# Kernel tuning notes

Hardware: AMD Instinct MI355X
Metric: run time of the kernel (lower is better)

## Reference

```python
import jax, jax.numpy as jnp
import numpy as np

N_NODES = 100000
N_EDGES = 3200000
IN_F = 256
OUT_F = 128


def setup_inputs() -> dict:
    key = jax.random.key(0)
    k1, k2, k3, k4, k5, k6 = jax.random.split(key, 6)
    x = jax.random.normal(k1, (N_NODES, IN_F), dtype=jnp.float32)
    edge_row = jax.random.randint(k2, (N_EDGES,), 0, N_NODES, dtype=jnp.int32)
    edge_col = jax.random.randint(k3, (N_EDGES,), 0, N_NODES, dtype=jnp.int32)
    edge_val = jax.random.uniform(k4, (N_EDGES,), dtype=jnp.float32)
    # xavier_uniform with relu gain, as in reset_parameters
    gain = float(np.sqrt(2.0))
    bound = gain * float(np.sqrt(6.0 / (IN_F + OUT_F)))
    w = jax.random.uniform(k5, (IN_F, OUT_F), minval=-bound, maxval=bound, dtype=jnp.float32)
    std = 1.0 / float(np.sqrt(OUT_F))
    bias = jax.random.uniform(k6, (OUT_F,), minval=-std, maxval=std, dtype=jnp.float32)
    return {"x": x, "edge_row": edge_row, "edge_col": edge_col,
            "edge_val": edge_val, "w": w, "bias": bias}


def reference(x, edge_row, edge_col, edge_val, w, bias):
    # h = x @ w : dense feature transform [N, out]
    h = jnp.matmul(x, w)
    # spmm(adj, h): out[r] = sum_e adj_val[e] * h[c[e]] for edges e with row r
    msgs = edge_val[:, None] * h[edge_col]  # [E, out]
    agg = jax.ops.segment_sum(msgs, edge_row, num_segments=N_NODES)
    return agg + bias
```

## Files before the change

### kernel.cpp

```cpp
#include <hip/hip_runtime.h>
#include <hip/hip_bf16.h>

#define N_NODES 100000
#define N_EDGES 3200000
#define IN_F 256
#define OUT_F 128

#define NBIN 391
#define NBC  800
#define CHUNK 4000
#define GEMM_BLOCKS 782

typedef __attribute__((ext_vector_type(8))) short bf16x8;
typedef __attribute__((ext_vector_type(4))) float f32x4;

union U4BF { uint4 u; bf16x8 v; };

__device__ inline unsigned short f2bf(float f) {
    return __bfloat16_as_ushort(__float2bfloat16(f));
}
__device__ inline unsigned pk2(float a, float b) {
    unsigned la = __bfloat16_as_ushort(__float2bfloat16(a));
    unsigned lb = __bfloat16_as_ushort(__float2bfloat16(b));
    return la | (lb << 16);
}

__global__ __launch_bounds__(256) void conv_w_kernel(
    const float* __restrict__ w, uint4* __restrict__ wbfF)
{
    int tid = blockIdx.x * 256 + threadIdx.x;
    int ks = tid >> 9;
    int fn = (tid >> 6) & 7;
    int l  = tid & 63;
    int c  = fn * 16 + (l & 15);
    int k0 = ks * 32 + (l >> 4) * 8;
    const float* wp = w + (size_t)k0 * OUT_F + c;
    uint4 u;
    u.x = pk2(wp[0 * OUT_F], wp[1 * OUT_F]);
    u.y = pk2(wp[2 * OUT_F], wp[3 * OUT_F]);
    u.z = pk2(wp[4 * OUT_F], wp[5 * OUT_F]);
    u.w = pk2(wp[6 * OUT_F], wp[7 * OUT_F]);
    wbfF[tid] = u;
}

__global__ __launch_bounds__(256) void gemm_hist_kernel(
    const float* __restrict__ x, const uint4* __restrict__ wbfF,
    unsigned short* __restrict__ h,
    const int* __restrict__ erow, int* __restrict__ cntmat)
{
    __shared__ __align__(16) char smem[65536];
    const int t = threadIdx.x;

    if (blockIdx.x < GEMM_BLOCKS) {
        uint4* bsh = (uint4*)smem;
        const int lane = t & 63;
        const int wid  = t >> 6;
        const int brow = blockIdx.x * 128;
        const int ln   = lane & 15;
        const int kb   = lane >> 4;

#pragma unroll
        for (int i = 0; i < 16; ++i) bsh[i * 256 + t] = wbfF[i * 256 + t];

        int r0 = brow + wid * 32 + ln;
        int r1 = r0 + 16;
        const float* a0p = x + (size_t)(r0 < N_NODES ? r0 : N_NODES - 1) * IN_F;
        const float* a1p = x + (size_t)(r1 < N_NODES ? r1 : N_NODES - 1) * IN_F;

        f32x4 acc[2][8] = {};
        __syncthreads();

#pragma unroll
        for (int ks = 0; ks < 8; ++ks) {
            const int k = ks * 32 + kb * 8;
            U4BF a0, a1;
            {
                float4 p = *(const float4*)(a0p + k);
                float4 q = *(const float4*)(a0p + k + 4);
                a0.u.x = pk2(p.x, p.y); a0.u.y = pk2(p.z, p.w);
                a0.u.z = pk2(q.x, q.y); a0.u.w = pk2(q.z, q.w);
            }
            {
                float4 p = *(const float4*)(a1p + k);
                float4 q = *(const float4*)(a1p + k + 4);
                a1.u.x = pk2(p.x, p.y); a1.u.y = pk2(p.z, p.w);
                a1.u.z = pk2(q.x, q.y); a1.u.w = pk2(q.z, q.w);
            }
            U4BF b[8];
#pragma unroll
            for (int fn = 0; fn < 8; ++fn)
                b[fn].u = bsh[(ks * 8 + fn) * 64 + lane];
#pragma unroll
            for (int fn = 0; fn < 8; ++fn) {
                acc[0][fn] = __builtin_amdgcn_mfma_f32_16x16x32_bf16(
                    a0.v, b[fn].v, acc[0][fn], 0, 0, 0);
                acc[1][fn] = __builtin_amdgcn_mfma_f32_16x16x32_bf16(
                    a1.v, b[fn].v, acc[1][fn], 0, 0, 0);
            }
        }

#pragma unroll
        for (int fm = 0; fm < 2; ++fm) {
#pragma unroll
            for (int r = 0; r < 4; ++r) {
                int grow = brow + wid * 32 + fm * 16 + (lane >> 4) * 4 + r;
                if (grow < N_NODES) {
                    unsigned short* dst = h + (size_t)grow * OUT_F + ln;
#pragma unroll
                    for (int fn = 0; fn < 8; ++fn)
                        dst[fn * 16] = f2bf(acc[fm][fn][r]);
                }
            }
        }
    } else {
        int* lhist = (int*)smem;
        const int b = blockIdx.x - GEMM_BLOCKS;
        for (int i = t; i < NBIN; i += 256) lhist[i] = 0;
        __syncthreads();

        const int base = b * CHUNK;
        const int end  = min(base + CHUNK, N_EDGES);
        for (int i = base + t * 4; i < end; i += 1024) {
            int4 r = *(const int4*)(erow + i);
            atomicAdd(&lhist[r.x >> 8], 1);
            atomicAdd(&lhist[r.y >> 8], 1);
            atomicAdd(&lhist[r.z >> 8], 1);
            atomicAdd(&lhist[r.w >> 8], 1);
        }
        __syncthreads();

        int* dst = cntmat + (size_t)b * NBIN;
        for (int j = t; j < NBIN; j += 256) dst[j] = lhist[j];
    }
}

__global__ __launch_bounds__(256) void pass_b_kernel(
    const int* __restrict__ cntmat, int* __restrict__ blockbase,
    int* __restrict__ tot)
{
    __shared__ int sh[256];
    const int t = threadIdx.x;
    const int j = blockIdx.x;
    int c[4];
    int ps = 0;
#pragma unroll
    for (int i = 0; i < 4; ++i) {
        int bb = 4 * t + i;
        c[i] = (bb < NBC) ? cntmat[(size_t)bb * NBIN + j] : 0;
        ps += c[i];
    }
    sh[t] = ps;
    __syncthreads();
    for (int off = 1; off < 256; off <<= 1) {
        int add = (t >= off) ? sh[t - off] : 0;
        __syncthreads();
        sh[t] += add;
        __syncthreads();
    }
    int excl = sh[t] - ps;
#pragma unroll
    for (int i = 0; i < 4; ++i) {
        int bb = 4 * t + i;
        if (bb < NBC) { blockbase[(size_t)bb * NBIN + j] = excl; excl += c[i]; }
    }
    if (t == 255) tot[j] = sh[255];
}

__global__ __launch_bounds__(512) void pass_b2_kernel(
    const int* __restrict__ tot, int* __restrict__ bucket_base)
{
    __shared__ int sh[512];
    const int t = threadIdx.x;
    int v = (t < NBIN) ? tot[t] : 0;
    sh[t] = v;
    __syncthreads();
    for (int off = 1; off < 512; off <<= 1) {
        int add = (t >= off) ? sh[t - off] : 0;
        __syncthreads();
        sh[t] += add;
        __syncthreads();
    }
    if (t < NBIN + 1) bucket_base[t] = sh[t] - v;
}

__global__ __launch_bounds__(256) void pass_c_kernel(
    const int* __restrict__ erow, const int* __restrict__ ecol,
    const float* __restrict__ eval_, const int* __restrict__ cntmat,
    const int* __restrict__ blockbase, const int* __restrict__ bucket_base,
    int2* __restrict__ tmp)
{
    __shared__ int2 skv[CHUNK];
    __shared__ int  sdelta[CHUNK];
    __shared__ int  cur[NBIN];
    __shared__ int  sdel[NBIN];
    __shared__ int  sscan[256];

    const int t = threadIdx.x;
    const int b = blockIdx.x;

    int j0 = 2 * t, j1 = 2 * t + 1;
    int c0 = (j0 < NBIN) ? cntmat[(size_t)b * NBIN + j0] : 0;
    int c1 = (j1 < NBIN) ? cntmat[(size_t)b * NBIN + j1] : 0;
    int ps = c0 + c1;
    sscan[t] = ps;
    __syncthreads();
    for (int off = 1; off < 256; off <<= 1) {
        int add = (t >= off) ? sscan[t - off] : 0;
        __syncthreads();
        sscan[t] += add;
        __syncthreads();
    }
    int excl = sscan[t] - ps;
    if (j0 < NBIN) {
        cur[j0]  = excl;
        sdel[j0] = bucket_base[j0] + blockbase[(size_t)b * NBIN + j0] - excl;
    }
    if (j1 < NBIN) {
        cur[j1]  = excl + c0;
        sdel[j1] = bucket_base[j1] + blockbase[(size_t)b * NBIN + j1] - (excl + c0);
    }
    __syncthreads();

    const int base = b * CHUNK;
    const int end  = min(base + CHUNK, N_EDGES);
    for (int i = base + t * 4; i < end; i += 1024) {
        int4   r = *(const int4*)(erow + i);
        int4   c = *(const int4*)(ecol + i);
        float4 v = *(const float4*)(eval_ + i);
        int bin, pos;
        bin = r.x >> 8; pos = atomicAdd(&cur[bin], 1);
        skv[pos] = make_int2(c.x | ((r.x & 255) << 17), __float_as_int(v.x));
        sdelta[pos] = sdel[bin];
        bin = r.y >> 8; pos = atomicAdd(&cur[bin], 1);
        skv[pos] = make_int2(c.y | ((r.y & 255) << 17), __float_as_int(v.y));
        sdelta[pos] = sdel[bin];
        bin = r.z >> 8; pos = atomicAdd(&cur[bin], 1);
        skv[pos] = make_int2(c.z | ((r.z & 255) << 17), __float_as_int(v.z));
        sdelta[pos] = sdel[bin];
        bin = r.w >> 8; pos = atomicAdd(&cur[bin], 1);
        skv[pos] = make_int2(c.w | ((r.w & 255) << 17), __float_as_int(v.w));
        sdelta[pos] = sdel[bin];
    }
    __syncthreads();

    const int n = end - base;
    for (int i = t; i < n; i += 256) {
        int2 kv = skv[i];
        tmp[sdelta[i] + i] = kv;
    }
}

__global__ __launch_bounds__(256) void pass_d_kernel(
    const int2* __restrict__ tmp, const int* __restrict__ bucket_base,
    int2* __restrict__ packed, int* __restrict__ row_start,
    int* __restrict__ rowtot)
{
    __shared__ int hist[256];
    __shared__ int cursor[256];
    const int t = threadIdx.x;
    const int j = blockIdx.x;
    const int base = bucket_base[j];
    const int end  = bucket_base[j + 1];

    hist[t] = 0;
    __syncthreads();

    for (int i = base + t; i < end; i += 256)
        atomicAdd(&hist[tmp[i].x >> 17], 1);
    __syncthreads();

    int hv = hist[t];
    cursor[t] = hv;
    __syncthreads();
    for (int off = 1; off < 256; off <<= 1) {
        int add = (t >= off) ? cursor[t - off] : 0;
        __syncthreads();
        cursor[t] += add;
        __syncthreads();
    }
    int excl = cursor[t] - hv;

    int r = j * 256 + t;
    if (r < N_NODES) {
        row_start[r] = base + excl;
        rowtot[r]    = hv;
    }
    __syncthreads();
    cursor[t] = excl;
    __syncthreads();

    for (int i = base + t; i < end; i += 256) {
        int2 p = tmp[i];
        int rl = p.x >> 17;
        int pos = atomicAdd(&cursor[rl], 1);
        packed[base + pos] = make_int2(p.x & 0x1FFFF, p.y);
    }
}

__global__ __launch_bounds__(256) void aggregate_kernel(
    const int2* __restrict__ packed, const int* __restrict__ row_start,
    const int* __restrict__ rowtot, const unsigned* __restrict__ h2,
    const float* __restrict__ bias, float* __restrict__ out)
{
    int wave = (blockIdx.x * 256 + threadIdx.x) >> 6;
    int lane = threadIdx.x & 63;
    if (wave >= N_NODES) return;

    int start = __builtin_amdgcn_readfirstlane(row_start[wave]);
    int deg   = __builtin_amdgcn_readfirstlane(rowtot[wave]);
    int end   = start + deg;

    const unsigned* hb = h2 + lane;
    float ax = 0.f, ay = 0.f;

    int e = start;
    for (; e + 7 < end; e += 8) {
        int2 p0 = packed[e];
        int2 p1 = packed[e + 1];
        int2 p2 = packed[e + 2];
        int2 p3 = packed[e + 3];
        int2 p4 = packed[e + 4];
        int2 p5 = packed[e + 5];
        int2 p6 = packed[e + 6];
        int2 p7 = packed[e + 7];
        unsigned u0 = hb[(size_t)p0.x << 6];
        unsigned u1 = hb[(size_t)p1.x << 6];
        unsigned u2 = hb[(size_t)p2.x << 6];
        unsigned u3 = hb[(size_t)p3.x << 6];
        unsigned u4 = hb[(size_t)p4.x << 6];
        unsigned u5 = hb[(size_t)p5.x << 6];
        unsigned u6 = hb[(size_t)p6.x << 6];
        unsigned u7 = hb[(size_t)p7.x << 6];
        float v0 = __int_as_float(p0.y), v1 = __int_as_float(p1.y);
        float v2 = __int_as_float(p2.y), v3 = __int_as_float(p3.y);
        float v4 = __int_as_float(p4.y), v5 = __int_as_float(p5.y);
        float v6 = __int_as_float(p6.y), v7 = __int_as_float(p7.y);
        ax = fmaf(v0, __uint_as_float(u0 << 16), ax);
        ay = fmaf(v0, __uint_as_float(u0 & 0xFFFF0000u), ay);
        ax = fmaf(v1, __uint_as_float(u1 << 16), ax);
        ay = fmaf(v1, __uint_as_float(u1 & 0xFFFF0000u), ay);
        ax = fmaf(v2, __uint_as_float(u2 << 16), ax);
        ay = fmaf(v2, __uint_as_float(u2 & 0xFFFF0000u), ay);
        ax = fmaf(v3, __uint_as_float(u3 << 16), ax);
        ay = fmaf(v3, __uint_as_float(u3 & 0xFFFF0000u), ay);
        ax = fmaf(v4, __uint_as_float(u4 << 16), ax);
        ay = fmaf(v4, __uint_as_float(u4 & 0xFFFF0000u), ay);
        ax = fmaf(v5, __uint_as_float(u5 << 16), ax);
        ay = fmaf(v5, __uint_as_float(u5 & 0xFFFF0000u), ay);
        ax = fmaf(v6, __uint_as_float(u6 << 16), ax);
        ay = fmaf(v6, __uint_as_float(u6 & 0xFFFF0000u), ay);
        ax = fmaf(v7, __uint_as_float(u7 << 16), ax);
        ay = fmaf(v7, __uint_as_float(u7 & 0xFFFF0000u), ay);
    }
    for (; e < end; ++e) {
        int2 p0 = packed[e];
        unsigned u0 = hb[(size_t)p0.x << 6];
        float v0 = __int_as_float(p0.y);
        ax = fmaf(v0, __uint_as_float(u0 << 16), ax);
        ay = fmaf(v0, __uint_as_float(u0 & 0xFFFF0000u), ay);
    }

    float2 b = *(const float2*)(bias + lane * 2);
    *(float2*)(out + (size_t)wave * OUT_F + lane * 2) = make_float2(ax + b.x, ay + b.y);
}

extern "C" void kernel_launch(void* const* d_in, const int* in_sizes, int n_in,
                              void* d_out, int out_size, void* d_ws, size_t ws_size,
                              hipStream_t stream)
{
    const float* x     = (const float*)d_in[0];
    const int*   erow  = (const int*)d_in[1];
    const int*   ecol  = (const int*)d_in[2];
    const float* eval_ = (const float*)d_in[3];
    const float* w     = (const float*)d_in[4];
    const float* bias  = (const float*)d_in[5];
    float*       out   = (float*)d_out;

    char* ws = (char*)d_ws;
    unsigned short* h           = (unsigned short*)(ws);
    int2*           tmp         = (int2*)(ws + 25600000);
    int2*           packed      = (int2*)(ws + 51200000);
    int*            cntmat      = (int*)(ws + 76800000);
    int*            blockbase   = (int*)(ws + 78051200);
    int*            tot         = (int*)(ws + 79302400);
    int*            bucket_base = (int*)(ws + 79303968);
    int*            row_start   = (int*)(ws + 79305536);
    int*            rowtot      = (int*)(ws + 79705536);
    uint4*          wbfF        = (uint4*)(ws + 80105536);

    hipLaunchKernelGGL(conv_w_kernel, dim3(16), dim3(256), 0, stream, w, wbfF);

    hipLaunchKernelGGL(gemm_hist_kernel, dim3(GEMM_BLOCKS + NBC), dim3(256), 0, stream,
                       x, wbfF, h, erow, cntmat);

    hipLaunchKernelGGL(pass_b_kernel, dim3(NBIN), dim3(256), 0, stream,
                       cntmat, blockbase, tot);
    hipLaunchKernelGGL(pass_b2_kernel, dim3(1), dim3(512), 0, stream, tot, bucket_base);

    hipLaunchKernelGGL(pass_c_kernel, dim3(NBC), dim3(256), 0, stream,
                       erow, ecol, eval_, cntmat, blockbase, bucket_base, tmp);

    hipLaunchKernelGGL(pass_d_kernel, dim3(NBIN), dim3(256), 0, stream,
                       tmp, bucket_base, packed, row_start, rowtot);

    hipLaunchKernelGGL(aggregate_kernel,
                       dim3((N_NODES * 64 + 255) / 256), dim3(256), 0, stream,
                       packed, row_start, rowtot, (const unsigned*)h, bias, out);
}
```

Measured before the change: 216.9 us.

## Fuse per-bucket row sort with aggregation using 64-row LDS buckets

The row-bucket width drops from 256 to 64 rows, with bin counts, chunk sizes and scan kernels resized to match. The final per-row counting sort and the SpMM aggregation are merged into one kernel. That kernel sorts each bucket's edges into LDS and gathers h rows straight from there, so the packed edge array and the row_start/rowtot arrays are no longer written to or read from global memory. The trade-offs are a fixed LDS capacity of 4096 edges per bucket with no overflow guard, and more bins in the histogram and scatter passes.

```diff
diff --git a/kernel.cpp b/kernel.cpp
--- a/kernel.cpp
+++ b/kernel.cpp
@@ -6,10 +6,13 @@
 #define IN_F 256
 #define OUT_F 128
 
-#define NBIN 391
-#define NBC  800
-#define CHUNK 4000
+#define RPB 64
+#define NBIN 1563
+#define NBC  1000
+#define CHUNK 3200
 #define GEMM_BLOCKS 782
+#define BPT 7
+#define CAP 4096
 
 typedef __attribute__((ext_vector_type(8))) short bf16x8;
 typedef __attribute__((ext_vector_type(4))) float f32x4;
@@ -122,10 +125,10 @@
         const int end  = min(base + CHUNK, N_EDGES);
         for (int i = base + t * 4; i < end; i += 1024) {
             int4 r = *(const int4*)(erow + i);
-            atomicAdd(&lhist[r.x >> 8], 1);
-            atomicAdd(&lhist[r.y >> 8], 1);
-            atomicAdd(&lhist[r.z >> 8], 1);
-            atomicAdd(&lhist[r.w >> 8], 1);
+            atomicAdd(&lhist[r.x >> 6], 1);
+            atomicAdd(&lhist[r.y >> 6], 1);
+            atomicAdd(&lhist[r.z >> 6], 1);
+            atomicAdd(&lhist[r.w >> 6], 1);
         }
         __syncthreads();
 
@@ -166,21 +169,26 @@
     if (t == 255) tot[j] = sh[255];
 }
 
-__global__ __launch_bounds__(512) void pass_b2_kernel(
+__global__ __launch_bounds__(1024) void pass_b2_kernel(
     const int* __restrict__ tot, int* __restrict__ bucket_base)
 {
-    __shared__ int sh[512];
+    __shared__ int sh[1024];
     const int t = threadIdx.x;
-    int v = (t < NBIN) ? tot[t] : 0;
-    sh[t] = v;
-    __syncthreads();
-    for (int off = 1; off < 512; off <<= 1) {
+    const int i0 = 2 * t, i1 = 2 * t + 1;
+    int v0 = (i0 < NBIN) ? tot[i0] : 0;
+    int v1 = (i1 < NBIN) ? tot[i1] : 0;
+    int ps = v0 + v1;
+    sh[t] = ps;
+    __syncthreads();
+    for (int off = 1; off < 1024; off <<= 1) {
         int add = (t >= off) ? sh[t - off] : 0;
         __syncthreads();
         sh[t] += add;
         __syncthreads();
     }
-    if (t < NBIN + 1) bucket_base[t] = sh[t] - v;
+    int excl = sh[t] - ps;
+    if (i0 <= NBIN) bucket_base[i0] = excl;
+    if (i1 <= NBIN) bucket_base[i1] = excl + v0;
 }
 
 __global__ __launch_bounds__(256) void pass_c_kernel(
@@ -190,7 +198,7 @@
     int2* __restrict__ tmp)
 {
     __shared__ int2 skv[CHUNK];
-    __shared__ int  sdelta[CHUNK];
+    __shared__ unsigned short sbin[CHUNK];
     __shared__ int  cur[NBIN];
     __shared__ int  sdel[NBIN];
     __shared__ int  sscan[256];
@@ -198,10 +206,14 @@
     const int t = threadIdx.x;
     const int b = blockIdx.x;
 
-    int j0 = 2 * t, j1 = 2 * t + 1;
-    int c0 = (j0 < NBIN) ? cntmat[(size_t)b * NBIN + j0] : 0;
-    int c1 = (j1 < NBIN) ? cntmat[(size_t)b * NBIN + j1] : 0;
-    int ps = c0 + c1;
+    int c[BPT];
+    int ps = 0;
+#pragma unroll
+    for (int i = 0; i < BPT; ++i) {
+        int bin = t * BPT + i;
+        c[i] = (bin < NBIN) ? cntmat[(size_t)b * NBIN + bin] : 0;
+        ps += c[i];
+    }
     sscan[t] = ps;
     __syncthreads();
     for (int off = 1; off < 256; off <<= 1) {
@@ -211,13 +223,14 @@
         __syncthreads();
     }
     int excl = sscan[t] - ps;
-    if (j0 < NBIN) {
-        cur[j0]  = excl;
-        sdel[j0] = bucket_base[j0] + blockbase[(size_t)b * NBIN + j0] - excl;
-    }
-    if (j1 < NBIN) {
-        cur[j1]  = excl + c0;
-        sdel[j1] = bucket_base[j1] + blockbase[(size_t)b * NBIN + j1] - (excl + c0);
+#pragma unroll
+    for (int i = 0; i < BPT; ++i) {
+        int bin = t * BPT + i;
+        if (bin < NBIN) {
+            cur[bin]  = excl;
+            sdel[bin] = bucket_base[bin] + blockbase[(size_t)b * NBIN + bin] - excl;
+            excl += c[i];
+        }
     }
     __syncthreads();
 
@@ -225,143 +238,132 @@
     const int end  = min(base + CHUNK, N_EDGES);
     for (int i = base + t * 4; i < end; i += 1024) {
         int4   r = *(const int4*)(erow + i);
-        int4   c = *(const int4*)(ecol + i);
+        int4   cc = *(const int4*)(ecol + i);
         float4 v = *(const float4*)(eval_ + i);
         int bin, pos;
-        bin = r.x >> 8; pos = atomicAdd(&cur[bin], 1);
-        skv[pos] = make_int2(c.x | ((r.x & 255) << 17), __float_as_int(v.x));
-        sdelta[pos] = sdel[bin];
-        bin = r.y >> 8; pos = atomicAdd(&cur[bin], 1);
-        skv[pos] = make_int2(c.y | ((r.y & 255) << 17), __float_as_int(v.y));
-        sdelta[pos] = sdel[bin];
-        bin = r.z >> 8; pos = atomicAdd(&cur[bin], 1);
-        skv[pos] = make_int2(c.z | ((r.z & 255) << 17), __float_as_int(v.z));
-        sdelta[pos] = sdel[bin];
-        bin = r.w >> 8; pos = atomicAdd(&cur[bin], 1);
-        skv[pos] = make_int2(c.w | ((r.w & 255) << 17), __float_as_int(v.w));
-        sdelta[pos] = sdel[bin];
+        bin = r.x >> 6; pos = atomicAdd(&cur[bin], 1);
+        skv[pos] = make_int2(cc.x | ((r.x & 63) << 17), __float_as_int(v.x));
+        sbin[pos] = (unsigned short)bin;
+        bin = r.y >> 6; pos = atomicAdd(&cur[bin], 1);
+        skv[pos] = make_int2(cc.y | ((r.y & 63) << 17), __float_as_int(v.y));
+        sbin[pos] = (unsigned short)bin;
+        bin = r.z >> 6; pos = atomicAdd(&cur[bin], 1);
+        skv[pos] = make_int2(cc.z | ((r.z & 63) << 17), __float_as_int(v.z));
+        sbin[pos] = (unsigned short)bin;
+        bin = r.w >> 6; pos = atomicAdd(&cur[bin], 1);
+        skv[pos] = make_int2(cc.w | ((r.w & 63) << 17), __float_as_int(v.w));
+        sbin[pos] = (unsigned short)bin;
     }
     __syncthreads();
 
     const int n = end - base;
     for (int i = t; i < n; i += 256) {
         int2 kv = skv[i];
-        tmp[sdelta[i] + i] = kv;
-    }
-}
-
-__global__ __launch_bounds__(256) void pass_d_kernel(
+        tmp[sdel[sbin[i]] + i] = kv;
+    }
+}
+
+__global__ __launch_bounds__(512) void fused_da_kernel(
     const int2* __restrict__ tmp, const int* __restrict__ bucket_base,
-    int2* __restrict__ packed, int* __restrict__ row_start,
-    int* __restrict__ rowtot)
-{
-    __shared__ int hist[256];
-    __shared__ int cursor[256];
-    const int t = threadIdx.x;
-    const int j = blockIdx.x;
+    const unsigned* __restrict__ h2, const float* __restrict__ bias,
+    float* __restrict__ out)
+{
+    __shared__ int2 skv[CAP];
+    __shared__ int  srow[RPB];
+    __shared__ int  scnt[RPB];
+    __shared__ int  cursor[RPB];
+
+    const int t    = threadIdx.x;
+    const int lane = t & 63;
+    const int w    = t >> 6;
+    const int j    = blockIdx.x;
     const int base = bucket_base[j];
-    const int end  = bucket_base[j + 1];
-
-    hist[t] = 0;
-    __syncthreads();
-
-    for (int i = base + t; i < end; i += 256)
-        atomicAdd(&hist[tmp[i].x >> 17], 1);
-    __syncthreads();
-
-    int hv = hist[t];
-    cursor[t] = hv;
-    __syncthreads();
-    for (int off = 1; off < 256; off <<= 1) {
-        int add = (t >= off) ? cursor[t - off] : 0;
-        __syncthreads();
-        cursor[t] += add;
-        __syncthreads();
-    }
-    int excl = cursor[t] - hv;
-
-    int r = j * 256 + t;
-    if (r < N_NODES) {
-        row_start[r] = base + excl;
-        rowtot[r]    = hv;
-    }
-    __syncthreads();
-    cursor[t] = excl;
-    __syncthreads();
-
-    for (int i = base + t; i < end; i += 256) {
-        int2 p = tmp[i];
+    const int n    = bucket_base[j + 1] - base;
+
+    if (t < RPB) cursor[t] = 0;
+    __syncthreads();
+    for (int i = t; i < n; i += 512)
+        atomicAdd(&cursor[tmp[base + i].x >> 17], 1);
+    __syncthreads();
+    if (t < RPB) { scnt[t] = cursor[t]; srow[t] = cursor[t]; }
+    __syncthreads();
+    for (int off = 1; off < RPB; off <<= 1) {
+        int add = (t >= off && t < RPB) ? srow[t - off] : 0;
+        __syncthreads();
+        if (t < RPB) srow[t] += add;
+        __syncthreads();
+    }
+    if (t < RPB) { int ex = srow[t] - scnt[t]; srow[t] = ex; cursor[t] = ex; }
+    __syncthreads();
+
+    for (int i = t; i < n; i += 512) {
+        int2 p = tmp[base + i];
         int rl = p.x >> 17;
         int pos = atomicAdd(&cursor[rl], 1);
-        packed[base + pos] = make_int2(p.x & 0x1FFFF, p.y);
-    }
-}
-
-__global__ __launch_bounds__(256) void aggregate_kernel(
-    const int2* __restrict__ packed, const int* __restrict__ row_start,
-    const int* __restrict__ rowtot, const unsigned* __restrict__ h2,
-    const float* __restrict__ bias, float* __restrict__ out)
-{
-    int wave = (blockIdx.x * 256 + threadIdx.x) >> 6;
-    int lane = threadIdx.x & 63;
-    if (wave >= N_NODES) return;
-
-    int start = __builtin_amdgcn_readfirstlane(row_start[wave]);
-    int deg   = __builtin_amdgcn_readfirstlane(rowtot[wave]);
-    int end   = start + deg;
+        skv[pos] = make_int2(p.x & 0x1FFFF, p.y);
+    }
+    __syncthreads();
 
     const unsigned* hb = h2 + lane;
-    float ax = 0.f, ay = 0.f;
-
-    int e = start;
-    for (; e + 7 < end; e += 8) {
-        int2 p0 = packed[e];
-        int2 p1 = packed[e + 1];
-        int2 p2 = packed[e + 2];
-        int2 p3 = packed[e + 3];
-        int2 p4 = packed[e + 4];
-        int2 p5 = packed[e + 5];
-        int2 p6 = packed[e + 6];
-        int2 p7 = packed[e + 7];
-        unsigned u0 = hb[(size_t)p0.x << 6];
-        unsigned u1 = hb[(size_t)p1.x << 6];
-        unsigned u2 = hb[(size_t)p2.x << 6];
-        unsigned u3 = hb[(size_t)p3.x << 6];
-        unsigned u4 = hb[(size_t)p4.x << 6];
-        unsigned u5 = hb[(size_t)p5.x << 6];
-        unsigned u6 = hb[(size_t)p6.x << 6];
-        unsigned u7 = hb[(size_t)p7.x << 6];
-        float v0 = __int_as_float(p0.y), v1 = __int_as_float(p1.y);
-        float v2 = __int_as_float(p2.y), v3 = __int_as_float(p3.y);
-        float v4 = __int_as_float(p4.y), v5 = __int_as_float(p5.y);
-        float v6 = __int_as_float(p6.y), v7 = __int_as_float(p7.y);
-        ax = fmaf(v0, __uint_as_float(u0 << 16), ax);
-        ay = fmaf(v0, __uint_as_float(u0 & 0xFFFF0000u), ay);
-        ax = fmaf(v1, __uint_as_float(u1 << 16), ax);
-        ay = fmaf(v1, __uint_as_float(u1 & 0xFFFF0000u), ay);
-        ax = fmaf(v2, __uint_as_float(u2 << 16), ax);
-        ay = fmaf(v2, __uint_as_float(u2 & 0xFFFF0000u), ay);
-        ax = fmaf(v3, __uint_as_float(u3 << 16), ax);
-        ay = fmaf(v3, __uint_as_float(u3 & 0xFFFF0000u), ay);
-        ax = fmaf(v4, __uint_as_float(u4 << 16), ax);
-        ay = fmaf(v4, __uint_as_float(u4 & 0xFFFF0000u), ay);
-        ax = fmaf(v5, __uint_as_float(u5 << 16), ax);
-        ay = fmaf(v5, __uint_as_float(u5 & 0xFFFF0000u), ay);
-        ax = fmaf(v6, __uint_as_float(u6 << 16), ax);
-        ay = fmaf(v6, __uint_as_float(u6 & 0xFFFF0000u), ay);
-        ax = fmaf(v7, __uint_as_float(u7 << 16), ax);
-        ay = fmaf(v7, __uint_as_float(u7 & 0xFFFF0000u), ay);
-    }
-    for (; e < end; ++e) {
-        int2 p0 = packed[e];
-        unsigned u0 = hb[(size_t)p0.x << 6];
-        float v0 = __int_as_float(p0.y);
-        ax = fmaf(v0, __uint_as_float(u0 << 16), ax);
-        ay = fmaf(v0, __uint_as_float(u0 & 0xFFFF0000u), ay);
-    }
-
-    float2 b = *(const float2*)(bias + lane * 2);
-    *(float2*)(out + (size_t)wave * OUT_F + lane * 2) = make_float2(ax + b.x, ay + b.y);
+#pragma unroll 1
+    for (int rr = w * 8; rr < w * 8 + 8; ++rr) {
+        int gr = j * RPB + rr;
+        if (gr >= N_NODES) break;
+        int s = srow[rr];
+        int end = s + scnt[rr];
+        float ax = 0.f, ay = 0.f;
+
+        int e = s;
+        for (; e + 7 < end; e += 8) {
+            int2 p0 = skv[e];
+            int2 p1 = skv[e + 1];
+            int2 p2 = skv[e + 2];
+            int2 p3 = skv[e + 3];
+            int2 p4 = skv[e + 4];
+            int2 p5 = skv[e + 5];
+            int2 p6 = skv[e + 6];
+            int2 p7 = skv[e + 7];
+            unsigned u0 = hb[(size_t)p0.x << 6];
+            unsigned u1 = hb[(size_t)p1.x << 6];
+            unsigned u2 = hb[(size_t)p2.x << 6];
+            unsigned u3 = hb[(size_t)p3.x << 6];
+            unsigned u4 = hb[(size_t)p4.x << 6];
+            unsigned u5 = hb[(size_t)p5.x << 6];
+            unsigned u6 = hb[(size_t)p6.x << 6];
+            unsigned u7 = hb[(size_t)p7.x << 6];
+            float v0 = __int_as_float(p0.y), v1 = __int_as_float(p1.y);
+            float v2 = __int_as_float(p2.y), v3 = __int_as_float(p3.y);
+            float v4 = __int_as_float(p4.y), v5 = __int_as_float(p5.y);
+            float v6 = __int_as_float(p6.y), v7 = __int_as_float(p7.y);
+            ax = fmaf(v0, __uint_as_float(u0 << 16), ax);
+            ay = fmaf(v0, __uint_as_float(u0 & 0xFFFF0000u), ay);
+            ax = fmaf(v1, __uint_as_float(u1 << 16), ax);
+            ay = fmaf(v1, __uint_as_float(u1 & 0xFFFF0000u), ay);
+            ax = fmaf(v2, __uint_as_float(u2 << 16), ax);
+            ay = fmaf(v2, __uint_as_float(u2 & 0xFFFF0000u), ay);
+            ax = fmaf(v3, __uint_as_float(u3 << 16), ax);
+            ay = fmaf(v3, __uint_as_float(u3 & 0xFFFF0000u), ay);
+            ax = fmaf(v4, __uint_as_float(u4 << 16), ax);
+            ay = fmaf(v4, __uint_as_float(u4 & 0xFFFF0000u), ay);
+            ax = fmaf(v5, __uint_as_float(u5 << 16), ax);
+            ay = fmaf(v5, __uint_as_float(u5 & 0xFFFF0000u), ay);
+            ax = fmaf(v6, __uint_as_float(u6 << 16), ax);
+            ay = fmaf(v6, __uint_as_float(u6 & 0xFFFF0000u), ay);
+            ax = fmaf(v7, __uint_as_float(u7 << 16), ax);
+            ay = fmaf(v7, __uint_as_float(u7 & 0xFFFF0000u), ay);
+        }
+        for (; e < end; ++e) {
+            int2 p0 = skv[e];
+            unsigned u0 = hb[(size_t)p0.x << 6];
+            float v0 = __int_as_float(p0.y);
+            ax = fmaf(v0, __uint_as_float(u0 << 16), ax);
+            ay = fmaf(v0, __uint_as_float(u0 & 0xFFFF0000u), ay);
+        }
+
+        float2 bb = *(const float2*)(bias + lane * 2);
+        *(float2*)(out + (size_t)gr * OUT_F + lane * 2) =
+            make_float2(ax + bb.x, ay + bb.y);
+    }
 }
 
 extern "C" void kernel_launch(void* const* d_in, const int* in_sizes, int n_in,
@@ -379,14 +381,11 @@
     char* ws = (char*)d_ws;
     unsigned short* h           = (unsigned short*)(ws);
     int2*           tmp         = (int2*)(ws + 25600000);
-    int2*           packed      = (int2*)(ws + 51200000);
-    int*            cntmat      = (int*)(ws + 76800000);
-    int*            blockbase   = (int*)(ws + 78051200);
-    int*            tot         = (int*)(ws + 79302400);
-    int*            bucket_base = (int*)(ws + 79303968);
-    int*            row_start   = (int*)(ws + 79305536);
-    int*            rowtot      = (int*)(ws + 79705536);
-    uint4*          wbfF        = (uint4*)(ws + 80105536);
+    int*            cntmat      = (int*)(ws + 51200000);
+    int*            blockbase   = (int*)(ws + 57452000);
+    int*            tot         = (int*)(ws + 63704000);
+    int*            bucket_base = (int*)(ws + 63712000);
+    uint4*          wbfF        = (uint4*)(ws + 63720000);
 
     hipLaunchKernelGGL(conv_w_kernel, dim3(16), dim3(256), 0, stream, w, wbfF);
 
@@ -395,15 +394,11 @@
 
     hipLaunchKernelGGL(pass_b_kernel, dim3(NBIN), dim3(256), 0, stream,
                        cntmat, blockbase, tot);
-    hipLaunchKernelGGL(pass_b2_kernel, dim3(1), dim3(512), 0, stream, tot, bucket_base);
+    hipLaunchKernelGGL(pass_b2_kernel, dim3(1), dim3(1024), 0, stream, tot, bucket_base);
 
     hipLaunchKernelGGL(pass_c_kernel, dim3(NBC), dim3(256), 0, stream,
                        erow, ecol, eval_, cntmat, blockbase, bucket_base, tmp);
 
-    hipLaunchKernelGGL(pass_d_kernel, dim3(NBIN), dim3(256), 0, stream,
-                       tmp, bucket_base, packed, row_start, rowtot);
-
-    hipLaunchKernelGGL(aggregate_kernel,
-                       dim3((N_NODES * 64 + 255) / 256), dim3(256), 0, stream,
-                       packed, row_start, rowtot, (const unsigned*)h, bias, out);
-}
+    hipLaunchKernelGGL(fused_da_kernel, dim3(NBIN), dim3(512), 0, stream,
+                       tmp, bucket_base, (const unsigned*)h, bias, out);
+}
```

Result: no change. 217.9 us (+0.4%).
